# Performance work log

Hardware: AMD Instinct MI355X
Metric: run time of the kernel (lower is better)

## Reference

```python
import jax, jax.numpy as jnp
import numpy as np

N_IN = 10    # input_dim: x has 2**N_IN features
N_OUT = 10   # output_dim: output has 2**N_OUT features
RANK = 10
BATCH = 512
STD = 0.5


def setup_inputs() -> dict:
    key = jax.random.key(0)
    ks = jax.random.split(key, 5)
    x = jax.random.normal(ks[0], (BATCH, 2 ** N_IN), dtype=jnp.float32)
    # Stacked tensor-train cores; each core is (rank, 2, 2, rank) as in the torch module.
    input_cores = STD * jax.random.normal(ks[1], (N_IN, RANK, 2, 2, RANK), dtype=jnp.float32)
    output_cores = STD * jax.random.normal(ks[2], (N_OUT, RANK, 2, 2, RANK), dtype=jnp.float32)
    # central core is (2,)*(N_IN+N_OUT) in the original; stored here as the
    # equivalent (2**N_IN, 2**N_OUT) matrix (identical math, same memory layout).
    central_core = STD * jax.random.normal(ks[3], (2 ** N_IN, 2 ** N_OUT), dtype=jnp.float32)
    bias = STD * jax.random.normal(ks[4], (1, 2 ** N_OUT), dtype=jnp.float32)
    return {"x": x, "input_cores": input_cores, "output_cores": output_cores,
            "central_core": central_core, "bias": bias}


def reference(x, input_cores, output_cores, central_core, bias):
    # Tensor-wheel contraction with a fixed, precomputed path (replaces the
    # per-call greedy tensornetwork contractor). Exact same sum as the original.
    B = x.shape[0]
    n, r = input_cores.shape[0], input_cores.shape[1]
    m = output_cores.shape[0]

    # --- absorb x into the input-core chain ---
    # State S: (B, l0, C_acc, r_cur, Q_rem) where
    #   l0    = open left bond of input core 0 (closes the ring later)
    #   C_acc = accumulated central-core legs c_1..c_i (dim 2^i, c_1 most significant)
    #   Q_rem = remaining input bits of x (x bit 1 is most significant, matching reshape)
    S = jnp.einsum('bpq,lpcs->blcsq', x.reshape(B, 2, -1), input_cores[0])
    for i in range(1, n):
        _, l, C, rc, Q = S.shape
        S = S.reshape(B, l, C, rc, 2, Q // 2)
        S = jnp.einsum('blcrpq,rpds->blcdsq', S, input_cores[i]).reshape(B, l, 2 * C, r, Q // 2)
    S = S[..., 0]  # (B, l0, 2^n, r_n)

    # --- contract the central core over all input-side legs (dominant GEMM) ---
    U = jnp.einsum('blcr,cd->blrd', S, central_core)  # (B, l0, r_n, 2^m)

    # --- sweep through the output-core chain ---
    # State V: (B, l0, P_acc, r_cur, D_rem); P_acc accumulates free output legs
    # p_1..p_j (p_1 most significant), D_rem holds remaining central output legs.
    V = U.reshape(B, r, 1, r, 2 ** m)
    for j in range(m):
        _, l, P, rc, D = V.shape
        V = V.reshape(B, l, P, rc, 2, D // 2)
        V = jnp.einsum('blxrdq,rpds->blxpsq', V, output_cores[j]).reshape(B, l, 2 * P, r, D // 2)

    # --- close the ring: trace l0 (input core 0 left bond) with rgt_m ---
    out = jnp.einsum('blpl->bp', V[..., 0])  # (B, 2^m)
    return out + bias
```

## Files before the change

kernel.cpp:

```cpp
#include <hip/hip_runtime.h>
#include <cstdint>
#include <cstddef>


typedef __attribute__((ext_vector_type(8))) short short8;
typedef __attribute__((ext_vector_type(4))) float f32x4;

static __device__ __forceinline__ unsigned short f2bf(float f) {
  union { float f; unsigned int u; } v; v.f = f;
  unsigned int r = v.u + 0x7FFFu + ((v.u >> 16) & 1u);
  return (unsigned short)(r >> 16);
}
static __device__ __forceinline__ unsigned int pack2(float a, float b) {
  return (unsigned int)f2bf(a) | ((unsigned int)f2bf(b) << 16);
}

static __device__ __forceinline__ int shuf_in(int stg, int u, int dd) {
  if (stg == 0) return ((u >> 4) << 6) | (dd << 4) | ((u & 3) << 2) | ((u >> 2) & 3);
  if (stg == 1) return ((u >> 2) << 4) | (dd << 2) | (u & 3);
  return (u << 2) | dd;
}
static __device__ __forceinline__ int shuf_out(int stg, int u, int dd) {
  if (stg == 0) return (dd << 6) | ((u & 15) << 2) | (u >> 4);
  if (stg == 1) return ((u >> 4) << 6) | (dd << 4) | ((u & 3) << 2) | ((u >> 2) & 3);
  if (stg == 2) return ((u >> 2) << 4) | (dd << 2) | (u & 3);
  return (u << 2) | dd;
}

static __device__ __forceinline__ void zero_row(unsigned short* st, int row) {
  f32x4 z = {0.f, 0.f, 0.f, 0.f};
  char* p = (char*)st + row * 144;
  #pragma unroll
  for (int i = 0; i < 9; ++i) *(f32x4*)(p + i * 16) = z;
}

static __device__ __forceinline__ void mfma_stage(
    const unsigned short* st, const unsigned short* __restrict__ Bf,
    int abase, int lane, f32x4 acc[4][3]) {
  short8 af[4][2];
  #pragma unroll
  for (int rt = 0; rt < 4; ++rt) {
    af[rt][0] = *(const short8*)((const char*)st + abase + rt * 2304);
    af[rt][1] = *(const short8*)((const char*)st + abase + rt * 2304 + 64);
  }
  short8 bfr[3][2];
  #pragma unroll
  for (int nt = 0; nt < 3; ++nt) {
    bfr[nt][0] = *(const short8*)&Bf[(nt * 2 + 0) * 512 + lane * 8];
    bfr[nt][1] = *(const short8*)&Bf[(nt * 2 + 1) * 512 + lane * 8];
  }
  #pragma unroll
  for (int rt = 0; rt < 4; ++rt)
    #pragma unroll
    for (int nt = 0; nt < 3; ++nt) {
      f32x4 a = {0.f, 0.f, 0.f, 0.f};
      a = __builtin_amdgcn_mfma_f32_16x16x32_bf16(af[rt][0], bfr[nt][0], a, 0, 0, 0);
      a = __builtin_amdgcn_mfma_f32_16x16x32_bf16(af[rt][1], bfr[nt][1], a, 0, 0, 0);
      acc[rt][nt] = a;
    }
}

static __device__ __forceinline__ void write_stage_lds(
    unsigned short* st, const f32x4 acc[4][3], int w, int quad,
    const int* ddv, const int* sv, int stg, bool input_side) {
  #pragma unroll
  for (int rt = 0; rt < 4; ++rt) {
    const int u = w * 16 + rt * 4 + quad;
    #pragma unroll
    for (int nt = 0; nt < 3; ++nt) {
      if (sv[nt] < 10) {
        const int dd = ddv[nt];
        const int row = input_side ? shuf_in(stg, u, dd) : shuf_out(stg, u, dd);
        uint2 v;
        v.x = pack2(acc[rt][nt][0], acc[rt][nt][1]);
        v.y = pack2(acc[rt][nt][2], acc[rt][nt][3]);
        *(uint2*)((char*)st + row * 144 + sv[nt] * 8) = v;
      }
    }
  }
}

__global__ __launch_bounds__(256) void k0_prep(
    const float* __restrict__ ic, const float* __restrict__ oc,
    const float* __restrict__ cc, unsigned short* __restrict__ Bt,
    float* __restrict__ c2x, unsigned short* __restrict__ bf1,
    unsigned short* __restrict__ bf3, unsigned short* __restrict__ bf3l) {
  const int t = threadIdx.x;
  const int bx = blockIdx.x;
  if (bx < 1024) {
    const int dly = bx;
    const int D = (dly & 3) * 256 + ((dly >> 2) & 3) * 64 + (dly >> 4);
    const int uC = (t >> 2) * 16 + (t & 3);
    ushort4 pk;
    pk.x = f2bf(cc[(size_t)(uC + 0) * 1024 + D]);
    pk.y = f2bf(cc[(size_t)(uC + 4) * 1024 + D]);
    pk.z = f2bf(cc[(size_t)(uC + 8) * 1024 + D]);
    pk.w = f2bf(cc[(size_t)(uC + 12) * 1024 + D]);
    *(ushort4*)&Bt[(size_t)dly * 1024 + 4 * t] = pk;
  } else if (bx == 1024) {
    for (int idx = t; idx < 1600; idx += 256) {
      int L = idx / 160, rem = idx - L * 160;
      int w = rem / 40, r2 = rem - w * 40;
      int pi = r2 / 10, s = r2 - pi * 10;
      int p1 = pi >> 1, p2 = pi & 1, c1 = w >> 1, c2v = w & 1;
      float a = 0.f;
      for (int r1 = 0; r1 < 10; ++r1)
        a += ic[L * 40 + p1 * 20 + c1 * 10 + r1] *
             ic[400 + r1 * 40 + p2 * 20 + c2v * 10 + s];
      c2x[idx] = a;
    }
  } else if (bx == 1025) {
    for (int idx = t; idx < 12288; idx += 256) {
      int j = idx & 7, lane = (idx >> 3) & 63, kc = (idx >> 9) & 1;
      int g2 = idx >> 10, stg = g2 / 3, nt = g2 - stg * 3;
      int c15 = lane & 15, quad = lane >> 4;
      int n = nt * 16 + c15, dd = n / 12, s = n - dd * 12;
      int k = kc * 32 + quad * 8 + j, c = k >> 2, pi = k & 3;
      float v = 0.f;
      if (k < 40 && s < 10) {
        int p1 = pi >> 1, p2 = pi & 1, d1 = dd >> 1, d2 = dd & 1;
        const float* A = ic + (2 * stg + 2) * 400;
        const float* B = ic + (2 * stg + 3) * 400;
        for (int tt = 0; tt < 10; ++tt)
          v += A[c * 40 + p1 * 20 + d1 * 10 + tt] *
               B[tt * 40 + p2 * 20 + d2 * 10 + s];
      }
      bf1[idx] = f2bf(v);
    }
  } else if (bx == 1026) {
    for (int idx = t; idx < 12288; idx += 256) {
      int j = idx & 7, lane = (idx >> 3) & 63, kc = (idx >> 9) & 1;
      int g2 = idx >> 10, stg = g2 / 3, nt = g2 - stg * 3;
      int c15 = lane & 15, quad = lane >> 4;
      int n = nt * 16 + c15, dd = n / 12, s = n - dd * 12;
      int k = kc * 32 + quad * 8 + j, c = k >> 2, pi = k & 3;
      float v = 0.f;
      if (k < 40 && s < 10) {
        int d1 = pi >> 1, d2 = pi & 1, p1 = dd >> 1, p2 = dd & 1;
        const float* A = oc + (2 * stg) * 400;
        const float* B = oc + (2 * stg + 1) * 400;
        for (int tt = 0; tt < 10; ++tt)
          v += A[c * 40 + p1 * 20 + d1 * 10 + tt] *
               B[tt * 40 + p2 * 20 + d2 * 10 + s];
      }
      bf3[idx] = f2bf(v);
    }
  } else {
    for (int idx = t; idx < 10240; idx += 256) {
      int j = idx & 7, lane = (idx >> 3) & 63, kc = (idx >> 9) & 1, L = idx >> 10;
      int c15 = lane & 15, quad = lane >> 4;
      int k = kc * 32 + quad * 8 + j, c = k >> 2, pi = k & 3;
      float v = 0.f;
      if (k < 40 && c15 < 4) {
        int dd = c15, d1 = pi >> 1, d2 = pi & 1, p1 = dd >> 1, p2 = dd & 1;
        for (int tt = 0; tt < 10; ++tt)
          v += oc[8 * 400 + c * 40 + p1 * 20 + d1 * 10 + tt] *
               oc[9 * 400 + tt * 40 + p2 * 20 + d2 * 10 + L];
      }
      bf3l[idx] = f2bf(v);
    }
  }
}

__global__ __launch_bounds__(256, 4) void k1_insweep(
    const float* __restrict__ x, const float* __restrict__ c2x,
    const unsigned short* __restrict__ bf1, unsigned short* __restrict__ S) {
  __shared__ __align__(16) unsigned short st[256 * 72];
  const int t = threadIdx.x, bx = blockIdx.x;
  const int b = bx / 10, L = bx - b * 10;
  const int lane = t & 63, w = t >> 6;
  const int c15 = lane & 15, quad = lane >> 4;
  int ddv[3], sv[3];
  #pragma unroll
  for (int nt = 0; nt < 3; ++nt) {
    int n = nt * 16 + c15; ddv[nt] = n / 12; sv[nt] = n - ddv[nt] * 12;
  }
  const int abase = (w * 64 + c15) * 144 + quad * 16;
  {
    const int row = w * 64 + c15 * 4 + quad;
    zero_row(st, row);
    const float* xb = x + (size_t)b * 1024;
    const float* C2 = c2x + L * 160 + w * 40;
    float accx[4][10];
    #pragma unroll
    for (int g = 0; g < 4; ++g)
      #pragma unroll
      for (int s = 0; s < 10; ++s) accx[g][s] = 0.f;
    #pragma unroll
    for (int pi = 0; pi < 4; ++pi) {
      float xv[4];
      #pragma unroll
      for (int g = 0; g < 4; ++g) xv[g] = xb[pi * 256 + g * 64 + lane];
      #pragma unroll
      for (int s = 0; s < 10; ++s) {
        const float bv = C2[pi * 10 + s];
        #pragma unroll
        for (int g = 0; g < 4; ++g) accx[g][s] = fmaf(xv[g], bv, accx[g][s]);
      }
    }
    #pragma unroll
    for (int s = 0; s < 10; ++s) {
      uint2 v;
      v.x = pack2(accx[0][s], accx[1][s]);
      v.y = pack2(accx[2][s], accx[3][s]);
      *(uint2*)((char*)st + row * 144 + s * 8) = v;
    }
  }
  __syncthreads();
  f32x4 acc[4][3];
  #pragma unroll 1
  for (int stg = 0; stg < 4; ++stg) {
    mfma_stage(st, bf1 + stg * 3072, abase, lane, acc);
    if (stg < 3) {
      __syncthreads();
      write_stage_lds(st, acc, w, quad, ddv, sv, stg, true);
      __syncthreads();
    } else {
      #pragma unroll
      for (int rt = 0; rt < 4; ++rt) {
        const int u = w * 16 + rt * 4 + quad;
        #pragma unroll
        for (int nt = 0; nt < 3; ++nt) {
          if (sv[nt] < 10) {
            uint2 v;
            v.x = pack2(acc[rt][nt][0], acc[rt][nt][1]);
            v.y = pack2(acc[rt][nt][2], acc[rt][nt][3]);
            *(uint2*)&S[((size_t)(bx * 10 + sv[nt])) * 1024 + u * 16 + ddv[nt] * 4] = v;
          }
        }
      }
    }
  }
}

__global__ __launch_bounds__(256) void k2_gemm(
    const unsigned short* __restrict__ A,
    const unsigned short* __restrict__ B,
    unsigned short* __restrict__ U2a,
    unsigned short* __restrict__ U2b) {
  __shared__ __align__(16) unsigned short Atile[2 * 128 * 32];
  __shared__ __align__(16) unsigned short Btile[2 * 128 * 32];
  const int t = threadIdx.x, bx = blockIdx.x;
  const int xcd = bx & 7;
  const int i8 = bx >> 3;
  const int bm = i8 & 7;
  const int bn = (i8 >> 3) * 8 + xcd;
  const int wave = t >> 6, lane = t & 63;
  const int wm = wave & 1, wn = wave >> 1;

  f32x4 acc[4][4];
  #pragma unroll
  for (int i = 0; i < 4; ++i)
    #pragma unroll
    for (int j = 0; j < 4; ++j) acc[i][j] = (f32x4){0.f, 0.f, 0.f, 0.f};

  const int arow = t >> 2, achk = t & 3;
  const unsigned short* Ag = A + (size_t)(bm * 128 + arow) * 1024 + achk * 8;
  const unsigned short* Bg = B + (size_t)(bn * 128 + arow) * 1024 + achk * 8;
  char* ldsA = (char*)Atile + wave * 1024;
  char* ldsB = (char*)Btile + wave * 1024;

  for (int k0 = 0; k0 < 1024; k0 += 64) {
    #pragma unroll
    for (int kk = 0; kk < 2; ++kk) {
      const int ko = k0 + kk * 32;
      __builtin_amdgcn_global_load_lds(
          (const __attribute__((address_space(1))) void*)(Ag + ko),
          (__attribute__((address_space(3))) void*)(ldsA + kk * 8192), 16, 0, 0);
      __builtin_amdgcn_global_load_lds(
          (const __attribute__((address_space(1))) void*)(Ag + 64 * 1024 + ko),
          (__attribute__((address_space(3))) void*)(ldsA + kk * 8192 + 4096), 16, 0, 0);
      __builtin_amdgcn_global_load_lds(
          (const __attribute__((address_space(1))) void*)(Bg + ko),
          (__attribute__((address_space(3))) void*)(ldsB + kk * 8192), 16, 0, 0);
      __builtin_amdgcn_global_load_lds(
          (const __attribute__((address_space(1))) void*)(Bg + 64 * 1024 + ko),
          (__attribute__((address_space(3))) void*)(ldsB + kk * 8192 + 4096), 16, 0, 0);
    }
    __syncthreads();
    const int kq = (lane >> 4) * 8;
    #pragma unroll
    for (int kk = 0; kk < 2; ++kk) {
      short8 af[4], bf[4];
      #pragma unroll
      for (int mt = 0; mt < 4; ++mt)
        af[mt] = *(const short8*)&Atile[kk * 4096 + (wm * 64 + mt * 16 + (lane & 15)) * 32 + kq];
      #pragma unroll
      for (int nt = 0; nt < 4; ++nt)
        bf[nt] = *(const short8*)&Btile[kk * 4096 + (wn * 64 + nt * 16 + (lane & 15)) * 32 + kq];
      #pragma unroll
      for (int mt = 0; mt < 4; ++mt)
        #pragma unroll
        for (int nt = 0; nt < 4; ++nt)
          acc[mt][nt] = __builtin_amdgcn_mfma_f32_16x16x32_bf16(
              af[mt], bf[nt], acc[mt][nt], 0, 0, 0);
    }
    __syncthreads();
  }
  const int quad = lane >> 4;
  const int col0 = bn * 128 + wn * 64 + (lane & 15);
  const int row0 = bm * 128 + wm * 64;
  #pragma unroll
  for (int nt = 0; nt < 4; ++nt) {
    const int n = col0 + nt * 16;
    const int bl = n / 10;
    const int r = n - bl * 10;
    char* dst = (r < 8)
        ? (char*)U2a + (size_t)bl * 16384 + (size_t)r * 8
        : (char*)U2b + (size_t)bl * 4096 + (size_t)(r - 8) * 8;
    const int rb = (r < 8) ? 64 : 16;
    #pragma unroll
    for (int mt = 0; mt < 4; ++mt) {
      const int mp = (row0 + mt * 16 + quad * 4) >> 2;
      uint2 v;
      v.x = pack2(acc[mt][nt][0], acc[mt][nt][1]);
      v.y = pack2(acc[mt][nt][2], acc[mt][nt][3]);
      *(uint2*)(dst + (size_t)mp * rb) = v;
    }
  }
}

__global__ __launch_bounds__(256, 4) void k3_outsweep(
    const unsigned short* __restrict__ U2a, const unsigned short* __restrict__ U2b,
    const unsigned short* __restrict__ bf3, const unsigned short* __restrict__ bf3l,
    const float* __restrict__ bias, float* __restrict__ out) {
  __shared__ __align__(16) unsigned short st[256 * 72];
  const int t = threadIdx.x, bx = blockIdx.x;
  const int b = bx / 10, L = bx - b * 10;
  const int lane = t & 63, w = t >> 6;
  const int c15 = lane & 15, quad = lane >> 4;
  int ddv[3], sv[3];
  #pragma unroll
  for (int nt = 0; nt < 3; ++nt) {
    int n = nt * 16 + c15; ddv[nt] = n / 12; sv[nt] = n - ddv[nt] * 12;
  }
  const int abase = (w * 64 + c15) * 144 + quad * 16;
  zero_row(st, t);
  __syncthreads();
  f32x4 acc[4][3];
  {
    short8 af[4][2], bfr[3][2];
    const char* Ua = (const char*)U2a + (size_t)bx * 16384;
    const char* Ub = (const char*)U2b + (size_t)bx * 4096;
    #pragma unroll
    for (int rt = 0; rt < 4; ++rt) {
      const int m = w * 64 + rt * 16 + c15;
      af[rt][0] = *(const short8*)(Ua + m * 64 + quad * 16);
      af[rt][1] = *(const short8*)(Ub + m * 16);
    }
    #pragma unroll
    for (int nt = 0; nt < 3; ++nt) {
      bfr[nt][0] = *(const short8*)&bf3[(nt * 2 + 0) * 512 + lane * 8];
      bfr[nt][1] = *(const short8*)&bf3[(nt * 2 + 1) * 512 + lane * 8];
    }
    #pragma unroll
    for (int rt = 0; rt < 4; ++rt)
      #pragma unroll
      for (int nt = 0; nt < 3; ++nt) {
        f32x4 a = {0.f, 0.f, 0.f, 0.f};
        a = __builtin_amdgcn_mfma_f32_16x16x32_bf16(af[rt][0], bfr[nt][0], a, 0, 0, 0);
        a = __builtin_amdgcn_mfma_f32_16x16x32_bf16(af[rt][1], bfr[nt][1], a, 0, 0, 0);
        acc[rt][nt] = a;
      }
    write_stage_lds(st, acc, w, quad, ddv, sv, 0, false);
    __syncthreads();
  }
  #pragma unroll 1
  for (int stg = 1; stg < 4; ++stg) {
    mfma_stage(st, bf3 + stg * 3072, abase, lane, acc);
    __syncthreads();
    write_stage_lds(st, acc, w, quad, ddv, sv, stg, false);
    __syncthreads();
  }
  {
    const unsigned short* Bf = bf3l + L * 1024;
    const short8 b0 = *(const short8*)&Bf[lane * 8];
    const short8 b1 = *(const short8*)&Bf[512 + lane * 8];
    #pragma unroll
    for (int rt = 0; rt < 4; ++rt) {
      const short8 a0 = *(const short8*)((const char*)st + abase + rt * 2304);
      const short8 a1 = *(const short8*)((const char*)st + abase + rt * 2304 + 64);
      f32x4 a = {0.f, 0.f, 0.f, 0.f};
      a = __builtin_amdgcn_mfma_f32_16x16x32_bf16(a0, b0, a, 0, 0, 0);
      a = __builtin_amdgcn_mfma_f32_16x16x32_bf16(a1, b1, a, 0, 0, 0);
      if (c15 < 4) {
        const int u = w * 16 + rt * 4 + quad;
        #pragma unroll
        for (int i = 0; i < 4; ++i) {
          const int idx = u * 16 + i * 4 + c15;
          float v = a[i];
          if (L == 0) v += bias[idx];
          atomicAdd(&out[(size_t)b * 1024 + idx], v);
        }
      }
    }
  }
}

extern "C" void kernel_launch(void* const* d_in, const int* in_sizes, int n_in,
                              void* d_out, int out_size, void* d_ws, size_t ws_size,
                              hipStream_t stream) {
  (void)in_sizes; (void)n_in; (void)ws_size;
  const float* x    = (const float*)d_in[0];
  const float* ic   = (const float*)d_in[1];
  const float* oc   = (const float*)d_in[2];
  const float* cc   = (const float*)d_in[3];
  const float* bias = (const float*)d_in[4];
  float* out = (float*)d_out;

  char* ws = (char*)d_ws;
  unsigned short* S    = (unsigned short*)(ws);
  unsigned short* U2a  = (unsigned short*)(ws + 104857600);
  unsigned short* U2b  = (unsigned short*)(ws + 188743680);
  unsigned short* Bt   = (unsigned short*)(ws + 209715200);
  float*          c2x  = (float*)(ws + 211812352);
  unsigned short* bf1  = (unsigned short*)(ws + 211818752);
  unsigned short* bf3  = (unsigned short*)(ws + 211843328);
  unsigned short* bf3l = (unsigned short*)(ws + 211867904);

  hipMemsetAsync(d_out, 0, (size_t)out_size * sizeof(float), stream);
  k0_prep<<<1028, 256, 0, stream>>>(ic, oc, cc, Bt, c2x, bf1, bf3, bf3l);
  k1_insweep<<<5120, 256, 0, stream>>>(x, c2x, bf1, S);
  k2_gemm<<<3200, 256, 0, stream>>>(Bt, S, U2a, U2b);
  k3_outsweep<<<5120, 256, 0, stream>>>(U2a, U2b, bf3, bf3l, bias, out);
}
```

Measured before the change: 380.3 us.

## Run tensor-train sweep kernels as single-wave blocks without barriers

The input and output sweep kernels now use one 64-thread wave per block instead of four. Each wave handles all 16 M-tiles of a batch/rank slice, so every __syncthreads becomes a compiler-only memory fence. The LDS row stride shrinks from 144 to 88 bytes, with explicit zero padding and a small tail region, which cuts shared memory per block. The aim is to remove barrier stalls and let more blocks fit per CU. The cost is a 16x3 f32x4 accumulator array per lane, which raises register pressure and may lower occupancy.

```diff
diff --git a/kernel.cpp b/kernel.cpp
--- a/kernel.cpp
+++ b/kernel.cpp
@@ -5,6 +5,8 @@
 
 typedef __attribute__((ext_vector_type(8))) short short8;
 typedef __attribute__((ext_vector_type(4))) float f32x4;
+
+#define KFENCE asm volatile("" ::: "memory")
 
 static __device__ __forceinline__ unsigned short f2bf(float f) {
   union { float f; unsigned int u; } v; v.f = f;
@@ -27,56 +29,59 @@
   return (u << 2) | dd;
 }
 
-static __device__ __forceinline__ void zero_row(unsigned short* st, int row) {
-  f32x4 z = {0.f, 0.f, 0.f, 0.f};
-  char* p = (char*)st + row * 144;
-  #pragma unroll
-  for (int i = 0; i < 9; ++i) *(f32x4*)(p + i * 16) = z;
-}
-
-static __device__ __forceinline__ void mfma_stage(
+static __device__ __forceinline__ void sweep_compute(
     const unsigned short* st, const unsigned short* __restrict__ Bf,
-    int abase, int lane, f32x4 acc[4][3]) {
-  short8 af[4][2];
-  #pragma unroll
-  for (int rt = 0; rt < 4; ++rt) {
-    af[rt][0] = *(const short8*)((const char*)st + abase + rt * 2304);
-    af[rt][1] = *(const short8*)((const char*)st + abase + rt * 2304 + 64);
-  }
+    int lane, int c15, int quad, f32x4 acc[16][3]) {
   short8 bfr[3][2];
   #pragma unroll
   for (int nt = 0; nt < 3; ++nt) {
     bfr[nt][0] = *(const short8*)&Bf[(nt * 2 + 0) * 512 + lane * 8];
     bfr[nt][1] = *(const short8*)&Bf[(nt * 2 + 1) * 512 + lane * 8];
   }
-  #pragma unroll
-  for (int rt = 0; rt < 4; ++rt)
+  const int abase = c15 * 88 + quad * 16;
+  #pragma unroll
+  for (int mt = 0; mt < 16; ++mt) {
+    const short8 a0 = *(const short8*)((const char*)st + mt * 1408 + abase);
+    const short8 a1 = *(const short8*)((const char*)st + mt * 1408 + abase + 64);
     #pragma unroll
     for (int nt = 0; nt < 3; ++nt) {
       f32x4 a = {0.f, 0.f, 0.f, 0.f};
-      a = __builtin_amdgcn_mfma_f32_16x16x32_bf16(af[rt][0], bfr[nt][0], a, 0, 0, 0);
-      a = __builtin_amdgcn_mfma_f32_16x16x32_bf16(af[rt][1], bfr[nt][1], a, 0, 0, 0);
-      acc[rt][nt] = a;
-    }
-}
-
-static __device__ __forceinline__ void write_stage_lds(
-    unsigned short* st, const f32x4 acc[4][3], int w, int quad,
-    const int* ddv, const int* sv, int stg, bool input_side) {
-  #pragma unroll
-  for (int rt = 0; rt < 4; ++rt) {
-    const int u = w * 16 + rt * 4 + quad;
+      a = __builtin_amdgcn_mfma_f32_16x16x32_bf16(a0, bfr[nt][0], a, 0, 0, 0);
+      a = __builtin_amdgcn_mfma_f32_16x16x32_bf16(a1, bfr[nt][1], a, 0, 0, 0);
+      acc[mt][nt] = a;
+    }
+  }
+}
+
+template <int STG, bool INPUT>
+static __device__ __forceinline__ void stage_writes(
+    unsigned short* st, const f32x4 acc[16][3], int quad,
+    const int* ddv, const int* sv) {
+  #pragma unroll
+  for (int mt = 0; mt < 16; ++mt) {
+    const int u = mt * 4 + quad;
     #pragma unroll
     for (int nt = 0; nt < 3; ++nt) {
       if (sv[nt] < 10) {
         const int dd = ddv[nt];
-        const int row = input_side ? shuf_in(stg, u, dd) : shuf_out(stg, u, dd);
+        const int row = INPUT ? shuf_in(STG, u, dd) : shuf_out(STG, u, dd);
         uint2 v;
-        v.x = pack2(acc[rt][nt][0], acc[rt][nt][1]);
-        v.y = pack2(acc[rt][nt][2], acc[rt][nt][3]);
-        *(uint2*)((char*)st + row * 144 + sv[nt] * 8) = v;
-      }
-    }
+        v.x = pack2(acc[mt][nt][0], acc[mt][nt][1]);
+        v.y = pack2(acc[mt][nt][2], acc[mt][nt][3]);
+        *(uint2*)((char*)st + row * 88 + sv[nt] * 8) = v;
+      }
+    }
+  }
+}
+
+static __device__ __forceinline__ void init_pad(unsigned short* st, int lane) {
+  uint2 z8 = {0u, 0u};
+  #pragma unroll
+  for (int g = 0; g < 4; ++g)
+    *(uint2*)((char*)st + (lane * 4 + g) * 88 + 80) = z8;
+  if (lane < 4) {
+    f32x4 z = {0.f, 0.f, 0.f, 0.f};
+    *(f32x4*)((char*)st + 22528 + lane * 16) = z;
   }
 }
 
@@ -162,72 +167,70 @@
   }
 }
 
-__global__ __launch_bounds__(256, 4) void k1_insweep(
+__global__ __launch_bounds__(64) void k1_insweep(
     const float* __restrict__ x, const float* __restrict__ c2x,
     const unsigned short* __restrict__ bf1, unsigned short* __restrict__ S) {
-  __shared__ __align__(16) unsigned short st[256 * 72];
-  const int t = threadIdx.x, bx = blockIdx.x;
+  __shared__ __align__(16) unsigned short st[11296];
+  const int lane = threadIdx.x, bx = blockIdx.x;
   const int b = bx / 10, L = bx - b * 10;
-  const int lane = t & 63, w = t >> 6;
   const int c15 = lane & 15, quad = lane >> 4;
   int ddv[3], sv[3];
   #pragma unroll
   for (int nt = 0; nt < 3; ++nt) {
     int n = nt * 16 + c15; ddv[nt] = n / 12; sv[nt] = n - ddv[nt] * 12;
   }
-  const int abase = (w * 64 + c15) * 144 + quad * 16;
+  init_pad(st, lane);
   {
-    const int row = w * 64 + c15 * 4 + quad;
-    zero_row(st, row);
     const float* xb = x + (size_t)b * 1024;
-    const float* C2 = c2x + L * 160 + w * 40;
-    float accx[4][10];
-    #pragma unroll
-    for (int g = 0; g < 4; ++g)
-      #pragma unroll
-      for (int s = 0; s < 10; ++s) accx[g][s] = 0.f;
-    #pragma unroll
-    for (int pi = 0; pi < 4; ++pi) {
-      float xv[4];
-      #pragma unroll
-      for (int g = 0; g < 4; ++g) xv[g] = xb[pi * 256 + g * 64 + lane];
+    #pragma unroll
+    for (int W = 0; W < 4; ++W) {
+      const float* C2 = c2x + L * 160 + W * 40;
+      float accx[4][10];
+      #pragma unroll
+      for (int g = 0; g < 4; ++g)
+        #pragma unroll
+        for (int s = 0; s < 10; ++s) accx[g][s] = 0.f;
+      #pragma unroll
+      for (int pi = 0; pi < 4; ++pi) {
+        float xv[4];
+        #pragma unroll
+        for (int g = 0; g < 4; ++g) xv[g] = xb[pi * 256 + g * 64 + lane];
+        #pragma unroll
+        for (int s = 0; s < 10; ++s) {
+          const float bv = C2[pi * 10 + s];
+          #pragma unroll
+          for (int g = 0; g < 4; ++g) accx[g][s] = fmaf(xv[g], bv, accx[g][s]);
+        }
+      }
+      const int row = W * 64 + c15 * 4 + quad;
       #pragma unroll
       for (int s = 0; s < 10; ++s) {
-        const float bv = C2[pi * 10 + s];
-        #pragma unroll
-        for (int g = 0; g < 4; ++g) accx[g][s] = fmaf(xv[g], bv, accx[g][s]);
-      }
-    }
-    #pragma unroll
-    for (int s = 0; s < 10; ++s) {
-      uint2 v;
-      v.x = pack2(accx[0][s], accx[1][s]);
-      v.y = pack2(accx[2][s], accx[3][s]);
-      *(uint2*)((char*)st + row * 144 + s * 8) = v;
-    }
-  }
-  __syncthreads();
-  f32x4 acc[4][3];
-  #pragma unroll 1
-  for (int stg = 0; stg < 4; ++stg) {
-    mfma_stage(st, bf1 + stg * 3072, abase, lane, acc);
-    if (stg < 3) {
-      __syncthreads();
-      write_stage_lds(st, acc, w, quad, ddv, sv, stg, true);
-      __syncthreads();
-    } else {
-      #pragma unroll
-      for (int rt = 0; rt < 4; ++rt) {
-        const int u = w * 16 + rt * 4 + quad;
-        #pragma unroll
-        for (int nt = 0; nt < 3; ++nt) {
-          if (sv[nt] < 10) {
-            uint2 v;
-            v.x = pack2(acc[rt][nt][0], acc[rt][nt][1]);
-            v.y = pack2(acc[rt][nt][2], acc[rt][nt][3]);
-            *(uint2*)&S[((size_t)(bx * 10 + sv[nt])) * 1024 + u * 16 + ddv[nt] * 4] = v;
-          }
-        }
+        uint2 v;
+        v.x = pack2(accx[0][s], accx[1][s]);
+        v.y = pack2(accx[2][s], accx[3][s]);
+        *(uint2*)((char*)st + row * 88 + s * 8) = v;
+      }
+    }
+  }
+  KFENCE;
+  f32x4 acc[16][3];
+  sweep_compute(st, bf1 + 0 * 3072, lane, c15, quad, acc);
+  KFENCE; stage_writes<0, true>(st, acc, quad, ddv, sv); KFENCE;
+  sweep_compute(st, bf1 + 1 * 3072, lane, c15, quad, acc);
+  KFENCE; stage_writes<1, true>(st, acc, quad, ddv, sv); KFENCE;
+  sweep_compute(st, bf1 + 2 * 3072, lane, c15, quad, acc);
+  KFENCE; stage_writes<2, true>(st, acc, quad, ddv, sv); KFENCE;
+  sweep_compute(st, bf1 + 3 * 3072, lane, c15, quad, acc);
+  #pragma unroll
+  for (int mt = 0; mt < 16; ++mt) {
+    const int u = mt * 4 + quad;
+    #pragma unroll
+    for (int nt = 0; nt < 3; ++nt) {
+      if (sv[nt] < 10) {
+        uint2 v;
+        v.x = pack2(acc[mt][nt][0], acc[mt][nt][1]);
+        v.y = pack2(acc[mt][nt][2], acc[mt][nt][3]);
+        *(uint2*)&S[((size_t)(bx * 10 + sv[nt])) * 1024 + u * 16 + ddv[nt] * 4] = v;
       }
     }
   }
@@ -320,71 +323,65 @@
   }
 }
 
-__global__ __launch_bounds__(256, 4) void k3_outsweep(
+__global__ __launch_bounds__(64) void k3_outsweep(
     const unsigned short* __restrict__ U2a, const unsigned short* __restrict__ U2b,
     const unsigned short* __restrict__ bf3, const unsigned short* __restrict__ bf3l,
     const float* __restrict__ bias, float* __restrict__ out) {
-  __shared__ __align__(16) unsigned short st[256 * 72];
-  const int t = threadIdx.x, bx = blockIdx.x;
+  __shared__ __align__(16) unsigned short st[11296];
+  const int lane = threadIdx.x, bx = blockIdx.x;
   const int b = bx / 10, L = bx - b * 10;
-  const int lane = t & 63, w = t >> 6;
   const int c15 = lane & 15, quad = lane >> 4;
   int ddv[3], sv[3];
   #pragma unroll
   for (int nt = 0; nt < 3; ++nt) {
     int n = nt * 16 + c15; ddv[nt] = n / 12; sv[nt] = n - ddv[nt] * 12;
   }
-  const int abase = (w * 64 + c15) * 144 + quad * 16;
-  zero_row(st, t);
-  __syncthreads();
-  f32x4 acc[4][3];
+  init_pad(st, lane);
+  f32x4 acc[16][3];
   {
-    short8 af[4][2], bfr[3][2];
-    const char* Ua = (const char*)U2a + (size_t)bx * 16384;
-    const char* Ub = (const char*)U2b + (size_t)bx * 4096;
-    #pragma unroll
-    for (int rt = 0; rt < 4; ++rt) {
-      const int m = w * 64 + rt * 16 + c15;
-      af[rt][0] = *(const short8*)(Ua + m * 64 + quad * 16);
-      af[rt][1] = *(const short8*)(Ub + m * 16);
-    }
+    short8 bfr[3][2];
     #pragma unroll
     for (int nt = 0; nt < 3; ++nt) {
       bfr[nt][0] = *(const short8*)&bf3[(nt * 2 + 0) * 512 + lane * 8];
       bfr[nt][1] = *(const short8*)&bf3[(nt * 2 + 1) * 512 + lane * 8];
     }
-    #pragma unroll
-    for (int rt = 0; rt < 4; ++rt)
+    const char* Ua = (const char*)U2a + (size_t)bx * 16384;
+    const char* Ub = (const char*)U2b + (size_t)bx * 4096;
+    #pragma unroll
+    for (int mt = 0; mt < 16; ++mt) {
+      const int m = mt * 16 + c15;
+      const short8 a0 = *(const short8*)(Ua + m * 64 + quad * 16);
+      const short8 a1 = *(const short8*)(Ub + m * 16);
       #pragma unroll
       for (int nt = 0; nt < 3; ++nt) {
         f32x4 a = {0.f, 0.f, 0.f, 0.f};
-        a = __builtin_amdgcn_mfma_f32_16x16x32_bf16(af[rt][0], bfr[nt][0], a, 0, 0, 0);
-        a = __builtin_amdgcn_mfma_f32_16x16x32_bf16(af[rt][1], bfr[nt][1], a, 0, 0, 0);
-        acc[rt][nt] = a;
-      }
-    write_stage_lds(st, acc, w, quad, ddv, sv, 0, false);
-    __syncthreads();
-  }
-  #pragma unroll 1
-  for (int stg = 1; stg < 4; ++stg) {
-    mfma_stage(st, bf3 + stg * 3072, abase, lane, acc);
-    __syncthreads();
-    write_stage_lds(st, acc, w, quad, ddv, sv, stg, false);
-    __syncthreads();
-  }
+        a = __builtin_amdgcn_mfma_f32_16x16x32_bf16(a0, bfr[nt][0], a, 0, 0, 0);
+        a = __builtin_amdgcn_mfma_f32_16x16x32_bf16(a1, bfr[nt][1], a, 0, 0, 0);
+        acc[mt][nt] = a;
+      }
+    }
+  }
+  KFENCE; stage_writes<0, false>(st, acc, quad, ddv, sv); KFENCE;
+  sweep_compute(st, bf3 + 1 * 3072, lane, c15, quad, acc);
+  KFENCE; stage_writes<1, false>(st, acc, quad, ddv, sv); KFENCE;
+  sweep_compute(st, bf3 + 2 * 3072, lane, c15, quad, acc);
+  KFENCE; stage_writes<2, false>(st, acc, quad, ddv, sv); KFENCE;
+  sweep_compute(st, bf3 + 3 * 3072, lane, c15, quad, acc);
+  KFENCE; stage_writes<3, false>(st, acc, quad, ddv, sv); KFENCE;
   {
     const unsigned short* Bf = bf3l + L * 1024;
     const short8 b0 = *(const short8*)&Bf[lane * 8];
     const short8 b1 = *(const short8*)&Bf[512 + lane * 8];
-    #pragma unroll
-    for (int rt = 0; rt < 4; ++rt) {
-      const short8 a0 = *(const short8*)((const char*)st + abase + rt * 2304);
-      const short8 a1 = *(const short8*)((const char*)st + abase + rt * 2304 + 64);
+    const int abase = c15 * 88 + quad * 16;
+    #pragma unroll
+    for (int mt = 0; mt < 16; ++mt) {
+      const short8 a0 = *(const short8*)((const char*)st + mt * 1408 + abase);
+      const short8 a1 = *(const short8*)((const char*)st + mt * 1408 + abase + 64);
       f32x4 a = {0.f, 0.f, 0.f, 0.f};
       a = __builtin_amdgcn_mfma_f32_16x16x32_bf16(a0, b0, a, 0, 0, 0);
       a = __builtin_amdgcn_mfma_f32_16x16x32_bf16(a1, b1, a, 0, 0, 0);
       if (c15 < 4) {
-        const int u = w * 16 + rt * 4 + quad;
+        const int u = mt * 4 + quad;
         #pragma unroll
         for (int i = 0; i < 4; ++i) {
           const int idx = u * 16 + i * 4 + c15;
@@ -420,7 +417,7 @@
 
   hipMemsetAsync(d_out, 0, (size_t)out_size * sizeof(float), stream);
   k0_prep<<<1028, 256, 0, stream>>>(ic, oc, cc, Bt, c2x, bf1, bf3, bf3l);
-  k1_insweep<<<5120, 256, 0, stream>>>(x, c2x, bf1, S);
+  k1_insweep<<<5120, 64, 0, stream>>>(x, c2x, bf1, S);
   k2_gemm<<<3200, 256, 0, stream>>>(Bt, S, U2a, U2b);
-  k3_outsweep<<<5120, 256, 0, stream>>>(U2a, U2b, bf3, bf3l, bias, out);
-}
+  k3_outsweep<<<5120, 64, 0, stream>>>(U2a, U2b, bf3, bf3l, bias, out);
+}
```

Result: slower. 535.5 us (+40.8%).

## Double-buffer LDS stages with compact 80-byte rows in sweep kernels

Applied to the files above, without the earlier changes.

The input and output sweep kernels now ping-pong between two LDS buffers instead of reusing one, which drops one __syncthreads per stage. The row stride shrinks from 144 to 80 bytes, so rows no longer carry zero padding. For lanes with quad≠0, the second MFMA A operand now reads arbitrary LDS data at offset 0 and relies on the B fragment being zero for k≥40 to cancel it. The stage loops are fully unrolled with templated stage indices so the shuffle arithmetic becomes compile-time. The cost is a slightly larger total LDS footprint per block (two buffers).

```diff
diff --git a/kernel.cpp b/kernel.cpp
--- a/kernel.cpp
+++ b/kernel.cpp
@@ -27,22 +27,9 @@
   return (u << 2) | dd;
 }
 
-static __device__ __forceinline__ void zero_row(unsigned short* st, int row) {
-  f32x4 z = {0.f, 0.f, 0.f, 0.f};
-  char* p = (char*)st + row * 144;
-  #pragma unroll
-  for (int i = 0; i < 9; ++i) *(f32x4*)(p + i * 16) = z;
-}
-
-static __device__ __forceinline__ void mfma_stage(
-    const unsigned short* st, const unsigned short* __restrict__ Bf,
-    int abase, int lane, f32x4 acc[4][3]) {
-  short8 af[4][2];
-  #pragma unroll
-  for (int rt = 0; rt < 4; ++rt) {
-    af[rt][0] = *(const short8*)((const char*)st + abase + rt * 2304);
-    af[rt][1] = *(const short8*)((const char*)st + abase + rt * 2304 + 64);
-  }
+static __device__ __forceinline__ void mfma_stage80(
+    const unsigned short* stc, const unsigned short* __restrict__ Bf,
+    int w, int lane, int c15, int quad, f32x4 acc[4][3]) {
   short8 bfr[3][2];
   #pragma unroll
   for (int nt = 0; nt < 3; ++nt) {
@@ -50,19 +37,25 @@
     bfr[nt][1] = *(const short8*)&Bf[(nt * 2 + 1) * 512 + lane * 8];
   }
   #pragma unroll
-  for (int rt = 0; rt < 4; ++rt)
+  for (int rt = 0; rt < 4; ++rt) {
+    const int rowA = w * 64 + rt * 16 + c15;
+    const short8 a0 = *(const short8*)((const char*)stc + rowA * 80 + quad * 16);
+    const int a1off = (quad == 0) ? rowA * 80 + 64 : 0;
+    const short8 a1 = *(const short8*)((const char*)stc + a1off);
     #pragma unroll
     for (int nt = 0; nt < 3; ++nt) {
       f32x4 a = {0.f, 0.f, 0.f, 0.f};
-      a = __builtin_amdgcn_mfma_f32_16x16x32_bf16(af[rt][0], bfr[nt][0], a, 0, 0, 0);
-      a = __builtin_amdgcn_mfma_f32_16x16x32_bf16(af[rt][1], bfr[nt][1], a, 0, 0, 0);
+      a = __builtin_amdgcn_mfma_f32_16x16x32_bf16(a0, bfr[nt][0], a, 0, 0, 0);
+      a = __builtin_amdgcn_mfma_f32_16x16x32_bf16(a1, bfr[nt][1], a, 0, 0, 0);
       acc[rt][nt] = a;
     }
-}
-
-static __device__ __forceinline__ void write_stage_lds(
-    unsigned short* st, const f32x4 acc[4][3], int w, int quad,
-    const int* ddv, const int* sv, int stg, bool input_side) {
+  }
+}
+
+template <int STG, bool INPUT>
+static __device__ __forceinline__ void stage_writes80(
+    unsigned short* dst, const f32x4 acc[4][3], int w, int quad,
+    const int* ddv, const int* sv) {
   #pragma unroll
   for (int rt = 0; rt < 4; ++rt) {
     const int u = w * 16 + rt * 4 + quad;
@@ -70,11 +63,11 @@
     for (int nt = 0; nt < 3; ++nt) {
       if (sv[nt] < 10) {
         const int dd = ddv[nt];
-        const int row = input_side ? shuf_in(stg, u, dd) : shuf_out(stg, u, dd);
+        const int row = INPUT ? shuf_in(STG, u, dd) : shuf_out(STG, u, dd);
         uint2 v;
         v.x = pack2(acc[rt][nt][0], acc[rt][nt][1]);
         v.y = pack2(acc[rt][nt][2], acc[rt][nt][3]);
-        *(uint2*)((char*)st + row * 144 + sv[nt] * 8) = v;
+        *(uint2*)((char*)dst + row * 80 + sv[nt] * 8) = v;
       }
     }
   }
@@ -165,7 +158,7 @@
 __global__ __launch_bounds__(256, 4) void k1_insweep(
     const float* __restrict__ x, const float* __restrict__ c2x,
     const unsigned short* __restrict__ bf1, unsigned short* __restrict__ S) {
-  __shared__ __align__(16) unsigned short st[256 * 72];
+  __shared__ __align__(16) unsigned short st[20480];
   const int t = threadIdx.x, bx = blockIdx.x;
   const int b = bx / 10, L = bx - b * 10;
   const int lane = t & 63, w = t >> 6;
@@ -175,10 +168,9 @@
   for (int nt = 0; nt < 3; ++nt) {
     int n = nt * 16 + c15; ddv[nt] = n / 12; sv[nt] = n - ddv[nt] * 12;
   }
-  const int abase = (w * 64 + c15) * 144 + quad * 16;
+  unsigned short* bufA = st;
+  unsigned short* bufB = st + 10240;
   {
-    const int row = w * 64 + c15 * 4 + quad;
-    zero_row(st, row);
     const float* xb = x + (size_t)b * 1024;
     const float* C2 = c2x + L * 160 + w * 40;
     float accx[4][10];
@@ -198,36 +190,37 @@
         for (int g = 0; g < 4; ++g) accx[g][s] = fmaf(xv[g], bv, accx[g][s]);
       }
     }
+    const int row = w * 64 + c15 * 4 + quad;
     #pragma unroll
     for (int s = 0; s < 10; ++s) {
       uint2 v;
       v.x = pack2(accx[0][s], accx[1][s]);
       v.y = pack2(accx[2][s], accx[3][s]);
-      *(uint2*)((char*)st + row * 144 + s * 8) = v;
+      *(uint2*)((char*)bufA + row * 80 + s * 8) = v;
     }
   }
   __syncthreads();
   f32x4 acc[4][3];
-  #pragma unroll 1
-  for (int stg = 0; stg < 4; ++stg) {
-    mfma_stage(st, bf1 + stg * 3072, abase, lane, acc);
-    if (stg < 3) {
-      __syncthreads();
-      write_stage_lds(st, acc, w, quad, ddv, sv, stg, true);
-      __syncthreads();
-    } else {
-      #pragma unroll
-      for (int rt = 0; rt < 4; ++rt) {
-        const int u = w * 16 + rt * 4 + quad;
-        #pragma unroll
-        for (int nt = 0; nt < 3; ++nt) {
-          if (sv[nt] < 10) {
-            uint2 v;
-            v.x = pack2(acc[rt][nt][0], acc[rt][nt][1]);
-            v.y = pack2(acc[rt][nt][2], acc[rt][nt][3]);
-            *(uint2*)&S[((size_t)(bx * 10 + sv[nt])) * 1024 + u * 16 + ddv[nt] * 4] = v;
-          }
-        }
+  mfma_stage80(bufA, bf1 + 0 * 3072, w, lane, c15, quad, acc);
+  stage_writes80<0, true>(bufB, acc, w, quad, ddv, sv);
+  __syncthreads();
+  mfma_stage80(bufB, bf1 + 1 * 3072, w, lane, c15, quad, acc);
+  stage_writes80<1, true>(bufA, acc, w, quad, ddv, sv);
+  __syncthreads();
+  mfma_stage80(bufA, bf1 + 2 * 3072, w, lane, c15, quad, acc);
+  stage_writes80<2, true>(bufB, acc, w, quad, ddv, sv);
+  __syncthreads();
+  mfma_stage80(bufB, bf1 + 3 * 3072, w, lane, c15, quad, acc);
+  #pragma unroll
+  for (int rt = 0; rt < 4; ++rt) {
+    const int u = w * 16 + rt * 4 + quad;
+    #pragma unroll
+    for (int nt = 0; nt < 3; ++nt) {
+      if (sv[nt] < 10) {
+        uint2 v;
+        v.x = pack2(acc[rt][nt][0], acc[rt][nt][1]);
+        v.y = pack2(acc[rt][nt][2], acc[rt][nt][3]);
+        *(uint2*)&S[((size_t)(bx * 10 + sv[nt])) * 1024 + u * 16 + ddv[nt] * 4] = v;
       }
     }
   }
@@ -324,7 +317,7 @@
     const unsigned short* __restrict__ U2a, const unsigned short* __restrict__ U2b,
     const unsigned short* __restrict__ bf3, const unsigned short* __restrict__ bf3l,
     const float* __restrict__ bias, float* __restrict__ out) {
-  __shared__ __align__(16) unsigned short st[256 * 72];
+  __shared__ __align__(16) unsigned short st[20480];
   const int t = threadIdx.x, bx = blockIdx.x;
   const int b = bx / 10, L = bx - b * 10;
   const int lane = t & 63, w = t >> 6;
@@ -334,52 +327,53 @@
   for (int nt = 0; nt < 3; ++nt) {
     int n = nt * 16 + c15; ddv[nt] = n / 12; sv[nt] = n - ddv[nt] * 12;
   }
-  const int abase = (w * 64 + c15) * 144 + quad * 16;
-  zero_row(st, t);
-  __syncthreads();
+  unsigned short* bufA = st;
+  unsigned short* bufB = st + 10240;
   f32x4 acc[4][3];
   {
-    short8 af[4][2], bfr[3][2];
-    const char* Ua = (const char*)U2a + (size_t)bx * 16384;
-    const char* Ub = (const char*)U2b + (size_t)bx * 4096;
-    #pragma unroll
-    for (int rt = 0; rt < 4; ++rt) {
-      const int m = w * 64 + rt * 16 + c15;
-      af[rt][0] = *(const short8*)(Ua + m * 64 + quad * 16);
-      af[rt][1] = *(const short8*)(Ub + m * 16);
-    }
+    short8 bfr[3][2];
     #pragma unroll
     for (int nt = 0; nt < 3; ++nt) {
       bfr[nt][0] = *(const short8*)&bf3[(nt * 2 + 0) * 512 + lane * 8];
       bfr[nt][1] = *(const short8*)&bf3[(nt * 2 + 1) * 512 + lane * 8];
     }
-    #pragma unroll
-    for (int rt = 0; rt < 4; ++rt)
+    const char* Ua = (const char*)U2a + (size_t)bx * 16384;
+    const char* Ub = (const char*)U2b + (size_t)bx * 4096;
+    #pragma unroll
+    for (int rt = 0; rt < 4; ++rt) {
+      const int m = w * 64 + rt * 16 + c15;
+      const short8 a0 = *(const short8*)(Ua + m * 64 + quad * 16);
+      const short8 a1 = *(const short8*)(Ub + m * 16);
       #pragma unroll
       for (int nt = 0; nt < 3; ++nt) {
         f32x4 a = {0.f, 0.f, 0.f, 0.f};
-        a = __builtin_amdgcn_mfma_f32_16x16x32_bf16(af[rt][0], bfr[nt][0], a, 0, 0, 0);
-        a = __builtin_amdgcn_mfma_f32_16x16x32_bf16(af[rt][1], bfr[nt][1], a, 0, 0, 0);
+        a = __builtin_amdgcn_mfma_f32_16x16x32_bf16(a0, bfr[nt][0], a, 0, 0, 0);
+        a = __builtin_amdgcn_mfma_f32_16x16x32_bf16(a1, bfr[nt][1], a, 0, 0, 0);
         acc[rt][nt] = a;
       }
-    write_stage_lds(st, acc, w, quad, ddv, sv, 0, false);
-    __syncthreads();
-  }
-  #pragma unroll 1
-  for (int stg = 1; stg < 4; ++stg) {
-    mfma_stage(st, bf3 + stg * 3072, abase, lane, acc);
-    __syncthreads();
-    write_stage_lds(st, acc, w, quad, ddv, sv, stg, false);
-    __syncthreads();
-  }
+    }
+    stage_writes80<0, false>(bufA, acc, w, quad, ddv, sv);
+  }
+  __syncthreads();
+  mfma_stage80(bufA, bf3 + 1 * 3072, w, lane, c15, quad, acc);
+  stage_writes80<1, false>(bufB, acc, w, quad, ddv, sv);
+  __syncthreads();
+  mfma_stage80(bufB, bf3 + 2 * 3072, w, lane, c15, quad, acc);
+  stage_writes80<2, false>(bufA, acc, w, quad, ddv, sv);
+  __syncthreads();
+  mfma_stage80(bufA, bf3 + 3 * 3072, w, lane, c15, quad, acc);
+  stage_writes80<3, false>(bufB, acc, w, quad, ddv, sv);
+  __syncthreads();
   {
     const unsigned short* Bf = bf3l + L * 1024;
     const short8 b0 = *(const short8*)&Bf[lane * 8];
     const short8 b1 = *(const short8*)&Bf[512 + lane * 8];
     #pragma unroll
     for (int rt = 0; rt < 4; ++rt) {
-      const short8 a0 = *(const short8*)((const char*)st + abase + rt * 2304);
-      const short8 a1 = *(const short8*)((const char*)st + abase + rt * 2304 + 64);
+      const int rowA = w * 64 + rt * 16 + c15;
+      const short8 a0 = *(const short8*)((const char*)bufB + rowA * 80 + quad * 16);
+      const int a1off = (quad == 0) ? rowA * 80 + 64 : 0;
+      const short8 a1 = *(const short8*)((const char*)bufB + a1off);
       f32x4 a = {0.f, 0.f, 0.f, 0.f};
       a = __builtin_amdgcn_mfma_f32_16x16x32_bf16(a0, b0, a, 0, 0, 0);
       a = __builtin_amdgcn_mfma_f32_16x16x32_bf16(a1, b1, a, 0, 0, 0);
@@ -387,10 +381,10 @@
         const int u = w * 16 + rt * 4 + quad;
         #pragma unroll
         for (int i = 0; i < 4; ++i) {
-          const int idx = u * 16 + i * 4 + c15;
+          const int oidx = u * 16 + i * 4 + c15;
           float v = a[i];
-          if (L == 0) v += bias[idx];
-          atomicAdd(&out[(size_t)b * 1024 + idx], v);
+          if (L == 0) v += bias[oidx];
+          atomicAdd(&out[(size_t)b * 1024 + oidx], v);
         }
       }
     }
```

Result: faster. 359.1 us (-5.6%).
